# Performance work log

Measured on AMD Instinct MI355X. Metric: run time of the kernel, lower is better.

## Reference

```python
import jax, jax.numpy as jnp
import numpy as np

D_MODEL = 1024
N_EXPERTS = 8
TOP_K = 2


def setup_inputs() -> dict:
    key = jax.random.key(0)
    ks = jax.random.split(key, 8)
    B, S, D, E, H = 4, 2048, D_MODEL, N_EXPERTS, 4 * D_MODEL
    s1 = 1.0 / np.sqrt(D)
    s2 = 1.0 / np.sqrt(H)
    return {
        "x": jax.random.normal(ks[0], (B, S, D), dtype=jnp.float32),
        "Wg": jax.random.uniform(ks[1], (D, E), jnp.float32, -s1, s1),
        "bg": jax.random.uniform(ks[2], (E,), jnp.float32, -s1, s1),
        "W1": jax.random.uniform(ks[3], (E, D, H), jnp.float32, -s1, s1),
        "b1": jax.random.uniform(ks[4], (E, H), jnp.float32, -s1, s1),
        "W2": jax.random.uniform(ks[5], (E, H, D), jnp.float32, -s2, s2),
        "b2": jax.random.uniform(ks[6], (E, D), jnp.float32, -s2, s2),
    }


def reference(x, Wg, bg, W1, b1, W2, b2):
    B, S, D = x.shape
    E = Wg.shape[1]
    x_flat = x.reshape(-1, D)                      # [T, D]
    logits = x_flat @ Wg + bg                      # [T, E]
    weights = jax.nn.softmax(logits, axis=-1)
    topk_w, topk_idx = jax.lax.top_k(weights, TOP_K)  # [T, K]
    # Per-token combine weight for each expert (sum over k where routed).
    onehot = jax.nn.one_hot(topk_idx, E, dtype=x.dtype)      # [T, K, E]
    combine = jnp.einsum("tk,tke->te", topk_w, onehot)       # [T, E]
    out = jnp.zeros_like(x_flat)
    for e in range(E):  # small fixed loop over experts
        h = jax.nn.gelu(x_flat @ W1[e] + b1[e], approximate=False)
        out = out + combine[:, e:e + 1] * (h @ W2[e] + b2[e])
    return out.reshape(B, S, D)
```

## Files before the change

### kernel.cpp

```cpp
#include <hip/hip_runtime.h>
#include <hip/hip_bf16.h>
#include <math.h>

#define T_TOK 8192
#define DM    1024
#define NE    8
#define HD    4096

typedef __bf16 bf16;
typedef __attribute__((ext_vector_type(8))) __bf16 bf16x8;
typedef __attribute__((ext_vector_type(4))) float  f32x4;

__device__ __forceinline__ void gl_lds16(const void* g, void* l) {
  __builtin_amdgcn_global_load_lds((const __attribute__((address_space(1))) void*)g,
                                   (__attribute__((address_space(3))) void*)l, 16, 0, 0);
}

#define RAW_BARRIER() asm volatile("s_barrier" ::: "memory")
#define VMCNT6()      asm volatile("s_waitcnt vmcnt(6)" ::: "memory")
#define VMCNT2()      asm volatile("s_waitcnt vmcnt(2)" ::: "memory")

__device__ __forceinline__ int imin(int a, int b) { return a < b ? a : b; }

__global__ void zero_kernel(float* __restrict__ out, int* __restrict__ counts) {
  size_t stride = (size_t)gridDim.x * blockDim.x;
  size_t n4 = (size_t)T_TOK * DM / 4;
  for (size_t i = (size_t)blockIdx.x * blockDim.x + threadIdx.x; i < n4; i += stride) {
    float4 z = {0.f, 0.f, 0.f, 0.f};
    ((float4*)out)[i] = z;
  }
  if (blockIdx.x == 0 && threadIdx.x < NE) counts[threadIdx.x] = 0;
}

__global__ void transpose_cvt_kernel(const float* __restrict__ in, bf16* __restrict__ out,
                                     int R, int C) {
  __shared__ float tile[64][65];
  int e = blockIdx.z;
  int c0 = blockIdx.x * 64, r0 = blockIdx.y * 64;
  int tid = threadIdx.x;
  int lr = tid >> 2, lc = (tid & 3) * 16;
  const float* src = in + ((size_t)e * R + r0 + lr) * C + c0 + lc;
#pragma unroll
  for (int q = 0; q < 4; ++q) {
    float4 v = *(const float4*)(src + q * 4);
    tile[lr][lc + q * 4 + 0] = v.x;
    tile[lr][lc + q * 4 + 1] = v.y;
    tile[lr][lc + q * 4 + 2] = v.z;
    tile[lr][lc + q * 4 + 3] = v.w;
  }
  __syncthreads();
  int oc = tid >> 3;
  int rchunk = tid & 7;
#pragma unroll
  for (int q = 0; q < 2; ++q) {
    int ocq = oc + q * 32;
    bf16x8 o;
#pragma unroll
    for (int k = 0; k < 8; ++k) o[k] = (bf16)tile[rchunk * 8 + k][ocq];
    *(bf16x8*)(out + ((size_t)e * C + c0 + ocq) * R + r0 + rchunk * 8) = o;
  }
}

__global__ void gating_kernel(const float* __restrict__ x, const float* __restrict__ Wg,
                              const float* __restrict__ bg, int* __restrict__ counts,
                              int* __restrict__ tokl, float* __restrict__ wgt,
                              bf16* __restrict__ xb) {
  int t = blockIdx.x * 4 + (threadIdx.x >> 6);
  int lane = threadIdx.x & 63;
  if (t >= T_TOK) return;
  double acc[NE];
#pragma unroll
  for (int e = 0; e < NE; ++e) acc[e] = 0.0;
  const float* xr = x + (size_t)t * DM;
  bf16* xbr = xb + (size_t)t * DM;
  for (int d = lane; d < DM; d += 64) {
    float xv = xr[d];
    xbr[d] = (bf16)xv;
#pragma unroll
    for (int e = 0; e < NE; ++e) acc[e] += (double)xv * (double)Wg[d * NE + e];
  }
#pragma unroll
  for (int e = 0; e < NE; ++e)
    for (int o = 32; o > 0; o >>= 1) acc[e] += __shfl_down(acc[e], o, 64);
  if (lane == 0) {
    float l[NE], w[NE];
    float m = -1e30f;
#pragma unroll
    for (int e = 0; e < NE; ++e) { l[e] = (float)acc[e] + bg[e]; m = fmaxf(m, l[e]); }
    float s = 0.f;
#pragma unroll
    for (int e = 0; e < NE; ++e) { w[e] = expf(l[e] - m); s += w[e]; }
    float inv = 1.f / s;
#pragma unroll
    for (int e = 0; e < NE; ++e) w[e] *= inv;
    int e1 = 0; float v1 = w[0];
#pragma unroll
    for (int e = 1; e < NE; ++e) if (w[e] > v1) { v1 = w[e]; e1 = e; }
    int e2 = -1; float v2 = -1.f;
#pragma unroll
    for (int e = 0; e < NE; ++e) if (e != e1 && w[e] > v2) { v2 = w[e]; e2 = e; }
    int s1 = atomicAdd(&counts[e1], 1);
    tokl[e1 * T_TOK + s1] = t; wgt[e1 * T_TOK + s1] = v1;
    int s2 = atomicAdd(&counts[e2], 1);
    tokl[e2 * T_TOK + s2] = t; wgt[e2 * T_TOK + s2] = v2;
  }
}

__global__ void scan_kernel(const int* __restrict__ counts, int* __restrict__ offsets) {
  if (threadIdx.x == 0 && blockIdx.x == 0) {
    int s = 0;
#pragma unroll
    for (int e = 0; e < NE; ++e) { offsets[e] = s; s += counts[e]; }
    offsets[NE] = s;
  }
}


#define LDA_F(IH, CB) \
  _Pragma("unroll") for (int kh = 0; kh < 2; ++kh) \
  _Pragma("unroll") for (int i = 0; i < 4; ++i) \
    af[kh*4+i] = *(const bf16x8*)(Ab + (CB) + (128*(IH) + 64*wm + 16*i + lf) * 128 + (colx ^ (kh*64)));

#define LDB_F(BF, JH, CB) \
  _Pragma("unroll") for (int kh = 0; kh < 2; ++kh) \
  _Pragma("unroll") for (int j = 0; j < 2; ++j) \
    BF[kh*2+j] = *(const bf16x8*)(Bb + (CB) + (128*(JH) + 32*wn + 16*j + lf) * 128 + (colx ^ (kh*64)));

#define MM_F(IH, JH, BF) \
  _Pragma("unroll") for (int kh = 0; kh < 2; ++kh) \
  _Pragma("unroll") for (int i = 0; i < 4; ++i) \
  _Pragma("unroll") for (int j = 0; j < 2; ++j) \
    acc[IH][JH][i][j] = __builtin_amdgcn_mfma_f32_16x16x32_bf16(af[kh*4+i], BF[kh*2+j], acc[IH][JH][i][j], 0, 0, 0);

#define ISSUE_A(H, NBO, KB) do { \
    gl_lds16(gA[2*(H)] + (KB), Al + (NBO) + (H)*16384 + dst); \
    gl_lds16(gA[2*(H)+1] + (KB), Al + (NBO) + (H)*16384 + 8192 + dst); \
  } while (0)
#define ISSUE_B(H, NBO, KB) do { \
    gl_lds16(gB[2*(H)] + (KB), Bl + (NBO) + (H)*16384 + dst); \
    gl_lds16(gB[2*(H)+1] + (KB), Bl + (NBO) + (H)*16384 + 8192 + dst); \
  } while (0)

#define KTILE_BODY(CB, NBO, KB) \
     \
    LDA_F(0, CB); \
    LDB_F(bfr0, 0, CB); \
    LDB_F(bfr1, 1, CB); \
    ISSUE_A(0, NBO, KB); \
    ISSUE_B(0, NBO, KB); \
    ISSUE_B(1, NBO, KB); \
    VMCNT6(); \
    RAW_BARRIER(); \
    __builtin_amdgcn_s_setprio(1); \
    MM_F(0, 0, bfr0); \
    MM_F(0, 1, bfr1); \
    __builtin_amdgcn_s_setprio(0); \
    RAW_BARRIER(); \
     \
    LDA_F(1, CB); \
    ISSUE_A(1, NBO, KB); \
    VMCNT2(); \
    RAW_BARRIER(); \
    __builtin_amdgcn_s_setprio(1); \
    MM_F(1, 0, bfr0); \
    MM_F(1, 1, bfr1); \
    __builtin_amdgcn_s_setprio(0); \
    RAW_BARRIER();

__global__ __launch_bounds__(512, 2) void gemm1_kernel(
    const bf16* __restrict__ xbf, const bf16* __restrict__ w1t,
    const float* __restrict__ b1, const int* __restrict__ counts,
    const int* __restrict__ offsets, const int* __restrict__ tokl,
    bf16* __restrict__ hbuf, int Hc, int cbase) {
  int bid = blockIdx.x;
  int q = gridDim.x >> 3;
  int L = (bid & 7) * q + (bid >> 3);
  int rt = L & 31;
  int g = L >> 5;
  int NT = Hc >> 8;
  int nt = g % NT, e = g / NT;
  int cnt = counts[e];
  if (rt * 256 >= cnt) return;
  __shared__ __align__(16) bf16 sA[2][256 * 64];
  __shared__ __align__(16) bf16 sB[2][256 * 64];
  int tid = threadIdx.x, lane = tid & 63, w = tid >> 6;
  int wm = w & 1, wn = w >> 1;
  int lf = lane & 15;
  int colx = ((lane >> 4) * 16) ^ ((lane & 7) << 4);
  int ra = tid >> 3;
  int ko = (tid & 7) * 16;
  int kox = ko ^ ((ra & 7) << 4);
  int dst = w * 1024;
  int hoff = offsets[e];
  const char* gA[4];
  const char* gB[4];
#pragma unroll
  for (int s = 0; s < 4; ++s) {
    int r = imin(rt * 256 + ra + s * 64, cnt - 1);
    int t = tokl[e * T_TOK + r];
    gA[s] = (const char*)(xbf + (size_t)t * DM) + kox;
    int col = cbase + nt * 256 + ra + s * 64;
    gB[s] = (const char*)(w1t + ((size_t)e * HD + col) * DM) + kox;
  }
  char* Al = (char*)sA;
  char* Bl = (char*)sB;
  const char* Ab = (const char*)sA;
  const char* Bb = (const char*)sB;
  f32x4 acc[2][2][4][2];
#pragma unroll
  for (int ih = 0; ih < 2; ++ih)
#pragma unroll
    for (int jh = 0; jh < 2; ++jh)
#pragma unroll
      for (int i = 0; i < 4; ++i)
#pragma unroll
        for (int j = 0; j < 2; ++j) acc[ih][jh][i][j] = {0.f, 0.f, 0.f, 0.f};
  bf16x8 af[8], bfr0[4], bfr1[4];
  const int K = DM / 64;
  ISSUE_A(0, 0, 0); ISSUE_B(0, 0, 0); ISSUE_B(1, 0, 0); ISSUE_A(1, 0, 0);
  VMCNT2();
  RAW_BARRIER();
  for (int k = 0; k < K; ++k) {
    int cb = (k & 1) * 32768;
    int nbo = ((k + 1) & 1) * 32768;
    int kb = (k + 1 < K) ? (k + 1) * 128 : 0;
    KTILE_BODY(cb, nbo, kb)
  }
  int colq = lane & 15, rowq = (lane >> 4) * 4;
  size_t ebase = (size_t)e * HD + cbase + nt * 256;
  float b1v[2][2];
#pragma unroll
  for (int jh = 0; jh < 2; ++jh)
#pragma unroll
    for (int j = 0; j < 2; ++j)
      b1v[jh][j] = b1[ebase + 128 * jh + 32 * wn + 16 * j + colq];
#pragma unroll
  for (int ih = 0; ih < 2; ++ih) {
#pragma unroll
    for (int i = 0; i < 4; ++i) {
#pragma unroll
      for (int r = 0; r < 4; ++r) {
        int grow = rt * 256 + 128 * ih + 64 * wm + 16 * i + rowq + r;
        if (grow < cnt) {
          size_t hrow = (size_t)(hoff + grow) * Hc + nt * 256;
#pragma unroll
          for (int jh = 0; jh < 2; ++jh) {
#pragma unroll
            for (int j = 0; j < 2; ++j) {
              float v = acc[ih][jh][i][j][r] + b1v[jh][j];
              float gl = 0.5f * v * (1.f + erff(v * 0.70710678118654752f));
              hbuf[hrow + 128 * jh + 32 * wn + 16 * j + colq] = (bf16)gl;
            }
          }
        }
      }
    }
  }
}

__global__ __launch_bounds__(512, 2) void gemm2_kernel(
    const bf16* __restrict__ hbuf, const bf16* __restrict__ w2t,
    const float* __restrict__ b2, const int* __restrict__ counts,
    const int* __restrict__ offsets, const int* __restrict__ tokl,
    const float* __restrict__ wgt, float* __restrict__ out,
    int Hc, int cbase, float b2scale) {
  int bid = blockIdx.x;
  int q = gridDim.x >> 3;
  int L = (bid & 7) * q + (bid >> 3);
  int rt = L & 31;
  int g = L >> 5;
  const int NT = DM / 256;
  int nt = g % NT, e = g / NT;
  int cnt = counts[e];
  if (rt * 256 >= cnt) return;
  __shared__ __align__(16) bf16 sA[2][256 * 64];
  __shared__ __align__(16) bf16 sB[2][256 * 64];
  int tid = threadIdx.x, lane = tid & 63, w = tid >> 6;
  int wm = w & 1, wn = w >> 1;
  int lf = lane & 15;
  int colx = ((lane >> 4) * 16) ^ ((lane & 7) << 4);
  int ra = tid >> 3;
  int ko = (tid & 7) * 16;
  int kox = ko ^ ((ra & 7) << 4);
  int dst = w * 1024;
  int hoff = offsets[e];
  const char* gA[4];
  const char* gB[4];
#pragma unroll
  for (int s = 0; s < 4; ++s) {
    int r = imin(rt * 256 + ra + s * 64, cnt - 1);
    gA[s] = (const char*)(hbuf + (size_t)(hoff + r) * Hc) + kox;
    int col = nt * 256 + ra + s * 64;
    gB[s] = (const char*)(w2t + ((size_t)e * DM + col) * HD + cbase) + kox;
  }
  char* Al = (char*)sA;
  char* Bl = (char*)sB;
  const char* Ab = (const char*)sA;
  const char* Bb = (const char*)sB;
  f32x4 acc[2][2][4][2];
#pragma unroll
  for (int ih = 0; ih < 2; ++ih)
#pragma unroll
    for (int jh = 0; jh < 2; ++jh)
#pragma unroll
      for (int i = 0; i < 4; ++i)
#pragma unroll
        for (int j = 0; j < 2; ++j) acc[ih][jh][i][j] = {0.f, 0.f, 0.f, 0.f};
  bf16x8 af[8], bfr0[4], bfr1[4];
  const int K = Hc / 64;
  ISSUE_A(0, 0, 0); ISSUE_B(0, 0, 0); ISSUE_B(1, 0, 0); ISSUE_A(1, 0, 0);
  VMCNT2();
  RAW_BARRIER();
  for (int k = 0; k < K; ++k) {
    int cb = (k & 1) * 32768;
    int nbo = ((k + 1) & 1) * 32768;
    int kb = (k + 1 < K) ? (k + 1) * 128 : 0;
    KTILE_BODY(cb, nbo, kb)
  }
  int colq = lane & 15, rowq = (lane >> 4) * 4;
  float b2v[2][2];
#pragma unroll
  for (int jh = 0; jh < 2; ++jh)
#pragma unroll
    for (int j = 0; j < 2; ++j)
      b2v[jh][j] = b2[(size_t)e * DM + nt * 256 + 128 * jh + 32 * wn + 16 * j + colq] * b2scale;
#pragma unroll
  for (int ih = 0; ih < 2; ++ih) {
#pragma unroll
    for (int i = 0; i < 4; ++i) {
#pragma unroll
      for (int r = 0; r < 4; ++r) {
        int grow = rt * 256 + 128 * ih + 64 * wm + 16 * i + rowq + r;
        if (grow < cnt) {
          float wv = wgt[e * T_TOK + grow];
          int tk = tokl[e * T_TOK + grow];
          float* orow = out + (size_t)tk * DM + nt * 256;
#pragma unroll
          for (int jh = 0; jh < 2; ++jh) {
#pragma unroll
            for (int j = 0; j < 2; ++j)
              atomicAdd(orow + 128 * jh + 32 * wn + 16 * j + colq,
                        wv * (acc[ih][jh][i][j][r] + b2v[jh][j]));
          }
        }
      }
    }
  }
}

extern "C" void kernel_launch(void* const* d_in, const int* in_sizes, int n_in,
                              void* d_out, int out_size, void* d_ws, size_t ws_size,
                              hipStream_t stream) {
  const float* x  = (const float*)d_in[0];
  const float* Wg = (const float*)d_in[1];
  const float* bg = (const float*)d_in[2];
  const float* W1 = (const float*)d_in[3];
  const float* b1 = (const float*)d_in[4];
  const float* W2 = (const float*)d_in[5];
  const float* b2 = (const float*)d_in[6];
  float* out = (float*)d_out;

  char* ws = (char*)d_ws;
  size_t off = 0;
  auto alloc = [&](size_t bytes) -> void* {
    void* p = ws + off;
    off = (off + bytes + 255) & ~(size_t)255;
    return p;
  };
  int*   counts  = (int*)alloc(NE * 4);
  int*   offsets = (int*)alloc((NE + 1) * 4);
  int*   tokl    = (int*)alloc((size_t)NE * T_TOK * 4);
  float* wgt     = (float*)alloc((size_t)NE * T_TOK * 4);
  bf16*  xbf     = (bf16*)alloc((size_t)T_TOK * DM * 2);
  bf16*  w1t     = (bf16*)alloc((size_t)NE * HD * DM * 2);
  bf16*  w2t     = (bf16*)alloc((size_t)NE * DM * HD * 2);
  size_t remain = ws_size > off ? ws_size - off : 0;
  int Hc = HD;
  while (Hc > 256 && (size_t)2 * T_TOK * Hc * 2 > remain) Hc >>= 1;
  bf16* hbuf = (bf16*)alloc((size_t)2 * T_TOK * Hc * 2);

  zero_kernel<<<4096, 256, 0, stream>>>(out, counts);
  transpose_cvt_kernel<<<dim3(HD / 64, DM / 64, NE), 256, 0, stream>>>(W1, w1t, DM, HD);
  transpose_cvt_kernel<<<dim3(DM / 64, HD / 64, NE), 256, 0, stream>>>(W2, w2t, HD, DM);
  gating_kernel<<<T_TOK / 4, 256, 0, stream>>>(x, Wg, bg, counts, tokl, wgt, xbf);
  scan_kernel<<<1, 64, 0, stream>>>(counts, offsets);

  int nchunk = HD / Hc;
  for (int c = 0; c < nchunk; ++c) {
    gemm1_kernel<<<NE * (Hc / 256) * (T_TOK / 256), 512, 0, stream>>>(
        xbf, w1t, b1, counts, offsets, tokl, hbuf, Hc, c * Hc);
    gemm2_kernel<<<NE * (DM / 256) * (T_TOK / 256), 512, 0, stream>>>(
        hbuf, w2t, b2, counts, offsets, tokl, wgt, out, Hc, c * Hc, c == 0 ? 1.f : 0.f);
  }
}
```

Baseline: 1.103 ms.

## Simplify GEMM k-loop to one barrier per tile with full prefetch upfront

Restructures the double-buffered k-loop of both expert GEMMs so all global-to-LDS loads for the next tile are issued at the start of the iteration. The loop now waits for them with vmcnt(0) and a single barrier at the end, replacing the staged vmcnt(6)/vmcnt(2) waits and four barriers per tile. It also skips the redundant prefetch on the last iteration. This cuts barrier synchronization overhead, but it drops the finer-grained interleaving of half-tile loads with compute and forces a full drain of outstanding loads every tile.

```diff
diff --git a/kernel.cpp b/kernel.cpp
--- a/kernel.cpp
+++ b/kernel.cpp
@@ -17,8 +17,7 @@
 }
 
 #define RAW_BARRIER() asm volatile("s_barrier" ::: "memory")
-#define VMCNT6()      asm volatile("s_waitcnt vmcnt(6)" ::: "memory")
-#define VMCNT2()      asm volatile("s_waitcnt vmcnt(2)" ::: "memory")
+#define VMCNT0()      asm volatile("s_waitcnt vmcnt(0)" ::: "memory")
 
 __device__ __forceinline__ int imin(int a, int b) { return a < b ? a : b; }
 
@@ -141,30 +140,24 @@
     gl_lds16(gB[2*(H)+1] + (KB), Bl + (NBO) + (H)*16384 + 8192 + dst); \
   } while (0)
 
-#define KTILE_BODY(CB, NBO, KB) \
-     \
+#define KTILE_BODY(CB, NBO, KB, STG) \
+    if (STG) { \
+      ISSUE_A(0, NBO, KB); ISSUE_B(0, NBO, KB); \
+      ISSUE_B(1, NBO, KB); ISSUE_A(1, NBO, KB); \
+    } \
     LDA_F(0, CB); \
     LDB_F(bfr0, 0, CB); \
     LDB_F(bfr1, 1, CB); \
-    ISSUE_A(0, NBO, KB); \
-    ISSUE_B(0, NBO, KB); \
-    ISSUE_B(1, NBO, KB); \
-    VMCNT6(); \
-    RAW_BARRIER(); \
     __builtin_amdgcn_s_setprio(1); \
     MM_F(0, 0, bfr0); \
     MM_F(0, 1, bfr1); \
     __builtin_amdgcn_s_setprio(0); \
-    RAW_BARRIER(); \
-     \
     LDA_F(1, CB); \
-    ISSUE_A(1, NBO, KB); \
-    VMCNT2(); \
-    RAW_BARRIER(); \
     __builtin_amdgcn_s_setprio(1); \
     MM_F(1, 0, bfr0); \
     MM_F(1, 1, bfr1); \
     __builtin_amdgcn_s_setprio(0); \
+    VMCNT0(); \
     RAW_BARRIER();
 
 __global__ __launch_bounds__(512, 2) void gemm1_kernel(
@@ -218,13 +211,13 @@
   bf16x8 af[8], bfr0[4], bfr1[4];
   const int K = DM / 64;
   ISSUE_A(0, 0, 0); ISSUE_B(0, 0, 0); ISSUE_B(1, 0, 0); ISSUE_A(1, 0, 0);
-  VMCNT2();
+  VMCNT0();
   RAW_BARRIER();
   for (int k = 0; k < K; ++k) {
     int cb = (k & 1) * 32768;
     int nbo = ((k + 1) & 1) * 32768;
-    int kb = (k + 1 < K) ? (k + 1) * 128 : 0;
-    KTILE_BODY(cb, nbo, kb)
+    int kb = (k + 1) * 128;
+    KTILE_BODY(cb, nbo, kb, (k + 1 < K))
   }
   int colq = lane & 15, rowq = (lane >> 4) * 4;
   size_t ebase = (size_t)e * HD + cbase + nt * 256;
@@ -309,13 +302,13 @@
   bf16x8 af[8], bfr0[4], bfr1[4];
   const int K = Hc / 64;
   ISSUE_A(0, 0, 0); ISSUE_B(0, 0, 0); ISSUE_B(1, 0, 0); ISSUE_A(1, 0, 0);
-  VMCNT2();
+  VMCNT0();
   RAW_BARRIER();
   for (int k = 0; k < K; ++k) {
     int cb = (k & 1) * 32768;
     int nbo = ((k + 1) & 1) * 32768;
-    int kb = (k + 1 < K) ? (k + 1) * 128 : 0;
-    KTILE_BODY(cb, nbo, kb)
+    int kb = (k + 1) * 128;
+    KTILE_BODY(cb, nbo, kb, (k + 1 < K))
   }
   int colq = lane & 15, rowq = (lane >> 4) * 4;
   float b2v[2][2];
```

New measurement: 1.140 ms. 1.03x slower.
